# Kernel optimization log

Measured on AMD Instinct MI355X. Metric: run time of the kernel, lower is better.

Reference implementation:

```python
import jax, jax.numpy as jnp
import numpy as np

N = 100000   # nodes
E = 1600000  # edges (avg degree 16)
IN = 7       # in_channels
H = 2        # heads
C = 64       # hidden_dim (per-head channels)
NC = 4       # num_classes
SLOPE = 0.2  # PyG GATConv default negative_slope


def gat_layer(x, W, a_src, a_dst, b, src, dst, concat):
    """PyG-style GATConv. x:[n,F], W:[F,H*C], a_*:[H,C], src/dst:[E'] (incl self-loops)."""
    n = x.shape[0]
    h = (x @ W).reshape(n, H, C)                 # [n,H,C]
    es = jnp.sum(h * a_src, axis=-1)             # [n,H] per-node source score
    ed = jnp.sum(h * a_dst, axis=-1)             # [n,H] per-node dest score
    e = jax.nn.leaky_relu(es[src] + ed[dst], SLOPE)          # [E',H]
    m = jax.ops.segment_max(e, dst, num_segments=n)          # stable segment softmax
    p = jnp.exp(e - m[dst])
    s = jax.ops.segment_sum(p, dst, num_segments=n)
    alpha = p / s[dst]                                        # [E',H]
    out = jax.ops.segment_sum(h[src] * alpha[:, :, None], dst, num_segments=n)  # [n,H,C]
    out = out.reshape(n, H * C) if concat else out.mean(axis=1)
    return out + b


def setup_inputs() -> dict:
    key = jax.random.key(0)
    ks = jax.random.split(key, 14)
    sc = 0.2
    return {
        "x": jax.random.normal(ks[0], (N, IN), jnp.float32),
        "edge_index": jax.random.randint(ks[1], (2, E), 0, N, dtype=jnp.int32),
        "W1": jax.random.normal(ks[2], (IN, H * C), jnp.float32) * sc,
        "a_src1": jax.random.normal(ks[3], (H, C), jnp.float32) * sc,
        "a_dst1": jax.random.normal(ks[4], (H, C), jnp.float32) * sc,
        "b1": jnp.zeros((H * C,), jnp.float32),
        "W2": jax.random.normal(ks[5], (H * C, H * C), jnp.float32) * sc,
        "a_src2": jax.random.normal(ks[6], (H, C), jnp.float32) * sc,
        "a_dst2": jax.random.normal(ks[7], (H, C), jnp.float32) * sc,
        "b2": jnp.zeros((C,), jnp.float32),
        "Wc1": jax.random.normal(ks[8], (C, C), jnp.float32) * sc,
        "bc1": jnp.zeros((C,), jnp.float32),
        "Wc2": jax.random.normal(ks[9], (C, NC), jnp.float32) * sc,
        "bc2": jnp.zeros((NC,), jnp.float32),
    }


def reference(x, edge_index, W1, a_src1, a_dst1, b1, W2, a_src2, a_dst2, b2, Wc1, bc1, Wc2, bc2):
    loops = jnp.arange(N, dtype=edge_index.dtype)            # PyG default add_self_loops=True
    src = jnp.concatenate([edge_index[0], loops])
    dst = jnp.concatenate([edge_index[1], loops])
    h = jax.nn.relu(gat_layer(x, W1, a_src1, a_dst1, b1, src, dst, True))   # [N, 128]
    h = gat_layer(h, W2, a_src2, a_dst2, b2, src, dst, False)               # [N, 64]
    return jax.nn.relu(h @ Wc1 + bc1) @ Wc2 + bc2                           # [N, 4]
```

## Files before the change

### kernel.cpp

```cpp
#include <hip/hip_runtime.h>
#include <hip/hip_bf16.h>


#define LRELU_SLOPE 0.2f

__device__ __forceinline__ float wave_red_max(float v) {
#pragma unroll
    for (int o = 32; o > 0; o >>= 1) v = fmaxf(v, __shfl_xor(v, o));
    return v;
}
__device__ __forceinline__ float wave_red_sum(float v) {
#pragma unroll
    for (int o = 32; o > 0; o >>= 1) v += __shfl_xor(v, o);
    return v;
}
__device__ __forceinline__ float lrelu(float v) { return v > 0.f ? v : LRELU_SLOPE * v; }
__device__ __forceinline__ unsigned short f2bf(float f) {
    unsigned int x = __float_as_uint(f);
    return (unsigned short)((x + 0x7fffu + ((x >> 16) & 1u)) >> 16);
}
__device__ __forceinline__ void fma8(float* f, uint4 hv, float a) {
    unsigned u[4] = {hv.x, hv.y, hv.z, hv.w};
#pragma unroll
    for (int i = 0; i < 4; i++) {
        float lo = __uint_as_float(u[i] << 16);
        float hi = __uint_as_float(u[i] & 0xffff0000u);
        f[2 * i]     += lo * a;
        f[2 * i + 1] += hi * a;
    }
}

__global__ void k_hist(const int* __restrict__ dstA, int* __restrict__ cnt, int E) {
    int i = blockIdx.x * 256 + threadIdx.x;
    if (i < E) atomicAdd(&cnt[dstA[i]], 1);
}

__global__ void k_scan1(const int* __restrict__ cnt, int* __restrict__ rs,
                        int* __restrict__ part, int n) {
    __shared__ int sm[256];
    int t = threadIdx.x;
    int i = blockIdx.x * 256 + t;
    int v = (i < n) ? cnt[i] : 0;
    sm[t] = v;
    __syncthreads();
#pragma unroll
    for (int off = 1; off < 256; off <<= 1) {
        int x = (t >= off) ? sm[t - off] : 0;
        __syncthreads();
        sm[t] += x;
        __syncthreads();
    }
    if (i < n) rs[i] = sm[t] - v;
    if (t == 255) part[blockIdx.x] = sm[255];
}

__global__ void k_scan2(int* part, int np) {
    __shared__ int sm[512];
    int t = threadIdx.x;
    int v = (t < np) ? part[t] : 0;
    sm[t] = v;
    __syncthreads();
#pragma unroll
    for (int off = 1; off < 512; off <<= 1) {
        int x = (t >= off) ? sm[t - off] : 0;
        __syncthreads();
        sm[t] += x;
        __syncthreads();
    }
    if (t < np) part[t] = sm[t] - v;
}

__global__ void k_scan3(int* rs, const int* __restrict__ part, int n, int total) {
    int i = blockIdx.x * 256 + threadIdx.x;
    if (i < n) rs[i] += part[blockIdx.x];
    if (i == 0) rs[n] = total;
}

__global__ void k_scatter(const int* __restrict__ srcA, const int* __restrict__ dstA,
                          const int* __restrict__ rs, int* __restrict__ cur,
                          int* __restrict__ ssrc, int E) {
    int i = blockIdx.x * 256 + threadIdx.x;
    if (i < E) {
        int d = dstA[i];
        int p = atomicAdd(&cur[d], 1);
        ssrc[rs[d] + p] = srcA[i];
    }
}

__global__ void k_prep(const float* __restrict__ W1, const float* __restrict__ as1,
                       const float* __restrict__ ad1, const float* __restrict__ W2,
                       const float* __restrict__ as2, const float* __restrict__ ad2,
                       float* __restrict__ ws1, float* __restrict__ wd1,
                       float* __restrict__ ws2, float* __restrict__ wd2) {
    int t = threadIdx.x;
    int k = t >> 1, h = t & 1;
    float s = 0.f, d = 0.f;
    for (int cc = 0; cc < 64; cc++) {
        float w = W2[k * 128 + h * 64 + cc];
        s += w * as2[h * 64 + cc];
        d += w * ad2[h * 64 + cc];
    }
    ws2[t] = s;
    wd2[t] = d;
    if (t < 14) {
        int kk = t >> 1, hh = t & 1;
        float s1 = 0.f, d1 = 0.f;
        for (int cc = 0; cc < 64; cc++) {
            float w = W1[kk * 128 + hh * 64 + cc];
            s1 += w * as1[hh * 64 + cc];
            d1 += w * ad1[hh * 64 + cc];
        }
        ws1[t] = s1;
        wd1[t] = d1;
    }
}

__global__ void k_feat1(const float* __restrict__ x, const float* __restrict__ W1,
                        const float* __restrict__ ws1, const float* __restrict__ wd1,
                        unsigned short* __restrict__ h1, float* __restrict__ es1,
                        float* __restrict__ ed1, int n) {
    int node = blockIdx.x;
    int c = threadIdx.x;
    float xv[7];
#pragma unroll
    for (int k = 0; k < 7; k++) xv[k] = x[node * 7 + k];
    float acc = 0.f;
#pragma unroll
    for (int k = 0; k < 7; k++) acc += xv[k] * W1[k * 128 + c];
    h1[(size_t)node * 128 + c] = f2bf(acc);
    if (c < 2) {
        float s = 0.f;
#pragma unroll
        for (int k = 0; k < 7; k++) s += xv[k] * ws1[k * 2 + c];
        es1[node * 2 + c] = s;
    } else if (c < 4) {
        int h = c - 2;
        float s = 0.f;
#pragma unroll
        for (int k = 0; k < 7; k++) s += xv[k] * wd1[k * 2 + h];
        ed1[node * 2 + h] = s;
    }
}

__global__ void k_alpha(const float* __restrict__ es, const float* __restrict__ ed,
                        const int* __restrict__ rs, const int* __restrict__ ssrc,
                        uint4* __restrict__ rec, float2* __restrict__ aself, int n) {
    int wid = threadIdx.x >> 6, lane = threadIdx.x & 63;
    int node = blockIdx.x * 4 + wid;
    if (node >= n) return;
    int beg = rs[node], deg = rs[node + 1] - beg;
    float2 edv = *(const float2*)&ed[node * 2];
    float2 esn = *(const float2*)&es[node * 2];
    float e0s = lrelu(esn.x + edv.x);
    float e1s = lrelu(esn.y + edv.y);

    if (deg <= 64) {
        bool valid = lane < deg;
        int sv = valid ? ssrc[beg + lane] : 0;
        float2 ev; ev.x = 0.f; ev.y = 0.f;
        if (valid) ev = *(const float2*)&es[sv * 2];
        float e0 = valid ? lrelu(ev.x + edv.x) : -3.0e38f;
        float e1 = valid ? lrelu(ev.y + edv.y) : -3.0e38f;
        float m0 = fmaxf(wave_red_max(e0), e0s);
        float m1 = fmaxf(wave_red_max(e1), e1s);
        float p0 = valid ? __expf(e0 - m0) : 0.f;
        float p1 = valid ? __expf(e1 - m1) : 0.f;
        float exs0 = __expf(e0s - m0), exs1 = __expf(e1s - m1);
        float inv0 = 1.f / (wave_red_sum(p0) + exs0);
        float inv1 = 1.f / (wave_red_sum(p1) + exs1);
        if (valid)
            rec[beg + lane] = make_uint4((unsigned)sv,
                                         __float_as_uint(p0 * inv0),
                                         __float_as_uint(p1 * inv1), 0u);
        if (lane == 0) {
            float2 a; a.x = exs0 * inv0; a.y = exs1 * inv1;
            aself[node] = a;
        }
    } else {
        float m0 = e0s, s0 = 1.f, m1 = e1s, s1 = 1.f;
        for (int c0 = 0; c0 < deg; c0 += 64) {
            int i = c0 + lane;
            bool val = i < deg;
            int sv = val ? ssrc[beg + i] : 0;
            float e0 = val ? lrelu(es[sv * 2 + 0] + edv.x) : -3.0e38f;
            float e1 = val ? lrelu(es[sv * 2 + 1] + edv.y) : -3.0e38f;
            float nm0 = fmaxf(m0, wave_red_max(e0));
            float nm1 = fmaxf(m1, wave_red_max(e1));
            float p0 = val ? __expf(e0 - nm0) : 0.f;
            float p1 = val ? __expf(e1 - nm1) : 0.f;
            s0 = s0 * __expf(m0 - nm0) + wave_red_sum(p0);
            s1 = s1 * __expf(m1 - nm1) + wave_red_sum(p1);
            m0 = nm0; m1 = nm1;
        }
        float inv0 = 1.f / s0, inv1 = 1.f / s1;
        for (int c0 = 0; c0 < deg; c0 += 64) {
            int i = c0 + lane;
            if (i < deg) {
                int sv = ssrc[beg + i];
                float e0 = lrelu(es[sv * 2 + 0] + edv.x);
                float e1 = lrelu(es[sv * 2 + 1] + edv.y);
                rec[beg + i] = make_uint4((unsigned)sv,
                                          __float_as_uint(__expf(e0 - m0) * inv0),
                                          __float_as_uint(__expf(e1 - m1) * inv1), 0u);
            }
        }
        if (lane == 0) {
            float2 a; a.x = __expf(e0s - m0) * inv0; a.y = __expf(e1s - m1) * inv1;
            aself[node] = a;
        }
    }
}

template <int LAYER>
__global__ void k_aggr(const unsigned short* __restrict__ h, const int* __restrict__ rs,
                       const uint4* __restrict__ rec, const float2* __restrict__ aself,
                       const float* __restrict__ bias, float* __restrict__ out,
                       const float* __restrict__ ws2, const float* __restrict__ wd2,
                       float* __restrict__ es2, float* __restrict__ ed2,
                       const float* __restrict__ Wc1, const float* __restrict__ bc1,
                       const float* __restrict__ Wc2, const float* __restrict__ bc2,
                       int n) {
    int wid = threadIdx.x >> 6, lane = threadIdx.x & 63;
    int node = blockIdx.x * 4 + wid;
    if (node >= n) return;
    int grp = lane >> 4, sub = lane & 15;
    int base = sub * 8;
    int hd = sub >> 3;
    int beg = rs[node], deg = rs[node + 1] - beg;
    float f[8] = {0.f, 0.f, 0.f, 0.f, 0.f, 0.f, 0.f, 0.f};

    if (grp == 0) {
        float2 as = aself[node];
        float a = hd ? as.y : as.x;
        uint4 hvs = *(const uint4*)&h[(size_t)node * 128 + base];
        fma8(f, hvs, a);
    }
    int j = grp;
    for (; j + 4 < deg; j += 8) {
        uint4 r0 = rec[beg + j];
        uint4 r1 = rec[beg + j + 4];
        uint4 h0 = *(const uint4*)&h[(size_t)(int)r0.x * 128 + base];
        uint4 h1v = *(const uint4*)&h[(size_t)(int)r1.x * 128 + base];
        fma8(f, h0, hd ? __uint_as_float(r0.z) : __uint_as_float(r0.y));
        fma8(f, h1v, hd ? __uint_as_float(r1.z) : __uint_as_float(r1.y));
    }
    if (j < deg) {
        uint4 r = rec[beg + j];
        uint4 hv = *(const uint4*)&h[(size_t)(int)r.x * 128 + base];
        fma8(f, hv, hd ? __uint_as_float(r.z) : __uint_as_float(r.y));
    }

#pragma unroll
    for (int r = 0; r < 8; r++) {
        f[r] += __shfl_xor(f[r], 16);
        f[r] += __shfl_xor(f[r], 32);
    }

    if (LAYER == 1) {
        float o[8];
#pragma unroll
        for (int r = 0; r < 8; r++) o[r] = fmaxf(f[r] + bias[base + r], 0.f);
        if (grp == 0) {
            float4 v0 = {o[0], o[1], o[2], o[3]};
            float4 v1 = {o[4], o[5], o[6], o[7]};
            *(float4*)&out[(size_t)node * 128 + base] = v0;
            *(float4*)&out[(size_t)node * 128 + base + 4] = v1;
        }
        float s0 = 0.f, s1 = 0.f, d0 = 0.f, d1 = 0.f;
#pragma unroll
        for (int r = 0; r < 8; r++) {
            float2 wsv = *(const float2*)&ws2[(base + r) * 2];
            float2 wdv = *(const float2*)&wd2[(base + r) * 2];
            s0 += o[r] * wsv.x; s1 += o[r] * wsv.y;
            d0 += o[r] * wdv.x; d1 += o[r] * wdv.y;
        }
        s0 = wave_red_sum(s0) * 0.25f;
        s1 = wave_red_sum(s1) * 0.25f;
        d0 = wave_red_sum(d0) * 0.25f;
        d1 = wave_red_sum(d1) * 0.25f;
        if (lane == 0) {
            float2 sv2; sv2.x = s0; sv2.y = s1;
            float2 dv2; dv2.x = d0; dv2.y = d1;
            *(float2*)&es2[node * 2] = sv2;
            *(float2*)&ed2[node * 2] = dv2;
        }
    } else {
        float p[8];
#pragma unroll
        for (int r = 0; r < 8; r++) p[r] = __shfl_xor(f[r], 8);
        float o2[8];
#pragma unroll
        for (int r = 0; r < 8; r++)
            o2[r] = 0.5f * (f[r] + p[r]) + bias[(base & 63) + r];
        float yc = bc1[lane];
#pragma unroll
        for (int k = 0; k < 64; k++) {
            float ov = __shfl(o2[k & 7], k >> 3);
            yc += ov * Wc1[k * 64 + lane];
        }
        float y = fmaxf(yc, 0.f);
        float4 w2v = *(const float4*)&Wc2[lane * 4];
        float p0 = y * w2v.x, p1 = y * w2v.y, p2 = y * w2v.z, p3 = y * w2v.w;
        p0 = wave_red_sum(p0); p1 = wave_red_sum(p1);
        p2 = wave_red_sum(p2); p3 = wave_red_sum(p3);
        if (lane == 0) {
            float4 o; o.x = p0 + bc2[0]; o.y = p1 + bc2[1];
            o.z = p2 + bc2[2]; o.w = p3 + bc2[3];
            *(float4*)&out[(size_t)node * 4] = o;
        }
    }
}

__global__ void k_gemm2(const float* __restrict__ A, const float* __restrict__ B,
                        unsigned short* __restrict__ C, int M) {
    __shared__ float As[32][65];
    __shared__ float Bs[32][132];
    int bm = blockIdx.x * 64;
    int t = threadIdx.x;
    int tx = t & 31;
    int ty = t >> 5;
    float acc[8][4];
#pragma unroll
    for (int i = 0; i < 8; i++)
#pragma unroll
        for (int j = 0; j < 4; j++) acc[i][j] = 0.f;

    for (int k0 = 0; k0 < 128; k0 += 32) {
        int lk = t & 31, lm = t >> 5;
#pragma unroll
        for (int p = 0; p < 8; p++) {
            int m = lm + p * 8;
            int row = bm + m;
            As[lk][m] = (row < M) ? A[(size_t)row * 128 + k0 + lk] : 0.f;
        }
        int bn = t & 127, bk = t >> 7;
#pragma unroll
        for (int p = 0; p < 16; p++) {
            Bs[bk + p * 2][bn] = B[(k0 + bk + p * 2) * 128 + bn];
        }
        __syncthreads();
#pragma unroll
        for (int k = 0; k < 32; k++) {
            float a[8];
#pragma unroll
            for (int i = 0; i < 8; i++) a[i] = As[k][ty * 8 + i];
            float4 bv = *(const float4*)&Bs[k][tx * 4];
            float b[4] = {bv.x, bv.y, bv.z, bv.w};
#pragma unroll
            for (int i = 0; i < 8; i++)
#pragma unroll
                for (int j = 0; j < 4; j++) acc[i][j] += a[i] * b[j];
        }
        __syncthreads();
    }
#pragma unroll
    for (int i = 0; i < 8; i++) {
        int row = bm + ty * 8 + i;
        if (row < M) {
            ushort4 v;
            v.x = f2bf(acc[i][0]); v.y = f2bf(acc[i][1]);
            v.z = f2bf(acc[i][2]); v.w = f2bf(acc[i][3]);
            *(ushort4*)&C[(size_t)row * 128 + tx * 4] = v;
        }
    }
}

extern "C" void kernel_launch(void* const* d_in, const int* in_sizes, int n_in,
                              void* d_out, int out_size, void* d_ws, size_t ws_size,
                              hipStream_t stream) {
    const float* x   = (const float*)d_in[0];
    const int*   ei  = (const int*)d_in[1];
    const float* W1  = (const float*)d_in[2];
    const float* as1 = (const float*)d_in[3];
    const float* ad1 = (const float*)d_in[4];
    const float* b1  = (const float*)d_in[5];
    const float* W2  = (const float*)d_in[6];
    const float* as2 = (const float*)d_in[7];
    const float* ad2 = (const float*)d_in[8];
    const float* b2  = (const float*)d_in[9];
    const float* Wc1 = (const float*)d_in[10];
    const float* bc1 = (const float*)d_in[11];
    const float* Wc2 = (const float*)d_in[12];
    const float* bc2 = (const float*)d_in[13];
    float* out = (float*)d_out;

    int n = in_sizes[0] / 7;
    int E = in_sizes[1] / 2;
    const int* srcA = ei;
    const int* dstA = ei + E;

    char* ws = (char*)d_ws;
    size_t off = 0;
    auto alloc = [&](size_t bytes) -> char* {
        char* p = ws + off;
        off += (bytes + 255) & ~(size_t)255;
        return p;
    };
    unsigned short* bufH = (unsigned short*)alloc((size_t)n * 128 * 2);
    float* bufO = (float*)alloc((size_t)n * 128 * 4);
    float* es1  = (float*)alloc((size_t)n * 2 * 4);
    float* ed1  = (float*)alloc((size_t)n * 2 * 4);
    float* es2  = (float*)alloc((size_t)n * 2 * 4);
    float* ed2  = (float*)alloc((size_t)n * 2 * 4);
    float* ws1  = (float*)alloc(64);
    float* wd1  = (float*)alloc(64);
    float* ws2v = (float*)alloc(256 * 4);
    float* wd2v = (float*)alloc(256 * 4);
    int* rs   = (int*)alloc((size_t)(n + 1) * 4);
    int* cnt  = (int*)alloc((size_t)n * 4);
    int* part = (int*)alloc(512 * 4);
    int* ssrc = (int*)alloc((size_t)E * 4);
    uint4* rec = (uint4*)alloc((size_t)E * 16);
    float2* aself = (float2*)alloc((size_t)n * 8);

    int eb = (E + 255) / 256;
    int nb = (n + 255) / 256;

    hipMemsetAsync(cnt, 0, (size_t)n * 4, stream);
    k_hist<<<eb, 256, 0, stream>>>(dstA, cnt, E);
    k_scan1<<<nb, 256, 0, stream>>>(cnt, rs, part, n);
    k_scan2<<<1, 512, 0, stream>>>(part, nb);
    k_scan3<<<nb, 256, 0, stream>>>(rs, part, n, E);
    hipMemsetAsync(cnt, 0, (size_t)n * 4, stream);
    k_scatter<<<eb, 256, 0, stream>>>(srcA, dstA, rs, cnt, ssrc, E);

    k_prep<<<1, 256, 0, stream>>>(W1, as1, ad1, W2, as2, ad2, ws1, wd1, ws2v, wd2v);
    k_feat1<<<n, 128, 0, stream>>>(x, W1, ws1, wd1, bufH, es1, ed1, n);
    k_alpha<<<(n + 3) / 4, 256, 0, stream>>>(es1, ed1, rs, ssrc, rec, aself, n);
    k_aggr<1><<<(n + 3) / 4, 256, 0, stream>>>(bufH, rs, rec, aself, b1, bufO,
                                               ws2v, wd2v, es2, ed2,
                                               nullptr, nullptr, nullptr, nullptr, n);
    k_gemm2<<<(n + 63) / 64, 256, 0, stream>>>(bufO, W2, bufH, n);
    k_alpha<<<(n + 3) / 4, 256, 0, stream>>>(es2, ed2, rs, ssrc, rec, aself, n);
    k_aggr<2><<<(n + 3) / 4, 256, 0, stream>>>(bufH, rs, rec, aself, b2, out,
                                               nullptr, nullptr, nullptr, nullptr,
                                               Wc1, bc1, Wc2, bc2, n);
}
```

Baseline: 625.6 us.

## Replace per-node softmax kernel with edge-parallel exp and deferred normalization

Removes the per-node k_alpha kernel, which did max/sum wave reductions and wrote normalized alphas. An edge-parallel k_edge kernel now writes unnormalized exp(leaky_relu) weights into CSR positions that k_scatter precomputes. k_aggr accumulates the weight sums alongside the features and divides once at the end. This drops the wave reductions and the per-node launch imbalance, and k_aggr gains a deeper 16-edge unroll. The trade-off is that without max subtraction, large attention logits could overflow exp, and the extra pos array plus srcA/dstA reads are added in each layer.

After: 597.9 us. -4.4%, faster.

```diff
diff --git a/kernel.cpp b/kernel.cpp
--- a/kernel.cpp
+++ b/kernel.cpp
@@ -4,11 +4,6 @@
 
 #define LRELU_SLOPE 0.2f
 
-__device__ __forceinline__ float wave_red_max(float v) {
-#pragma unroll
-    for (int o = 32; o > 0; o >>= 1) v = fmaxf(v, __shfl_xor(v, o));
-    return v;
-}
 __device__ __forceinline__ float wave_red_sum(float v) {
 #pragma unroll
     for (int o = 32; o > 0; o >>= 1) v += __shfl_xor(v, o);
@@ -76,14 +71,13 @@
     if (i == 0) rs[n] = total;
 }
 
-__global__ void k_scatter(const int* __restrict__ srcA, const int* __restrict__ dstA,
-                          const int* __restrict__ rs, int* __restrict__ cur,
-                          int* __restrict__ ssrc, int E) {
+__global__ void k_scatter(const int* __restrict__ dstA, const int* __restrict__ rs,
+                          int* __restrict__ cur, int* __restrict__ pos, int E) {
     int i = blockIdx.x * 256 + threadIdx.x;
     if (i < E) {
         int d = dstA[i];
         int p = atomicAdd(&cur[d], 1);
-        ssrc[rs[d] + p] = srcA[i];
+        pos[i] = rs[d] + p;
     }
 }
 
@@ -142,84 +136,29 @@
     }
 }
 
-__global__ void k_alpha(const float* __restrict__ es, const float* __restrict__ ed,
-                        const int* __restrict__ rs, const int* __restrict__ ssrc,
-                        uint4* __restrict__ rec, float2* __restrict__ aself, int n) {
-    int wid = threadIdx.x >> 6, lane = threadIdx.x & 63;
-    int node = blockIdx.x * 4 + wid;
-    if (node >= n) return;
-    int beg = rs[node], deg = rs[node + 1] - beg;
-    float2 edv = *(const float2*)&ed[node * 2];
-    float2 esn = *(const float2*)&es[node * 2];
-    float e0s = lrelu(esn.x + edv.x);
-    float e1s = lrelu(esn.y + edv.y);
-
-    if (deg <= 64) {
-        bool valid = lane < deg;
-        int sv = valid ? ssrc[beg + lane] : 0;
-        float2 ev; ev.x = 0.f; ev.y = 0.f;
-        if (valid) ev = *(const float2*)&es[sv * 2];
-        float e0 = valid ? lrelu(ev.x + edv.x) : -3.0e38f;
-        float e1 = valid ? lrelu(ev.y + edv.y) : -3.0e38f;
-        float m0 = fmaxf(wave_red_max(e0), e0s);
-        float m1 = fmaxf(wave_red_max(e1), e1s);
-        float p0 = valid ? __expf(e0 - m0) : 0.f;
-        float p1 = valid ? __expf(e1 - m1) : 0.f;
-        float exs0 = __expf(e0s - m0), exs1 = __expf(e1s - m1);
-        float inv0 = 1.f / (wave_red_sum(p0) + exs0);
-        float inv1 = 1.f / (wave_red_sum(p1) + exs1);
-        if (valid)
-            rec[beg + lane] = make_uint4((unsigned)sv,
-                                         __float_as_uint(p0 * inv0),
-                                         __float_as_uint(p1 * inv1), 0u);
-        if (lane == 0) {
-            float2 a; a.x = exs0 * inv0; a.y = exs1 * inv1;
-            aself[node] = a;
-        }
-    } else {
-        float m0 = e0s, s0 = 1.f, m1 = e1s, s1 = 1.f;
-        for (int c0 = 0; c0 < deg; c0 += 64) {
-            int i = c0 + lane;
-            bool val = i < deg;
-            int sv = val ? ssrc[beg + i] : 0;
-            float e0 = val ? lrelu(es[sv * 2 + 0] + edv.x) : -3.0e38f;
-            float e1 = val ? lrelu(es[sv * 2 + 1] + edv.y) : -3.0e38f;
-            float nm0 = fmaxf(m0, wave_red_max(e0));
-            float nm1 = fmaxf(m1, wave_red_max(e1));
-            float p0 = val ? __expf(e0 - nm0) : 0.f;
-            float p1 = val ? __expf(e1 - nm1) : 0.f;
-            s0 = s0 * __expf(m0 - nm0) + wave_red_sum(p0);
-            s1 = s1 * __expf(m1 - nm1) + wave_red_sum(p1);
-            m0 = nm0; m1 = nm1;
-        }
-        float inv0 = 1.f / s0, inv1 = 1.f / s1;
-        for (int c0 = 0; c0 < deg; c0 += 64) {
-            int i = c0 + lane;
-            if (i < deg) {
-                int sv = ssrc[beg + i];
-                float e0 = lrelu(es[sv * 2 + 0] + edv.x);
-                float e1 = lrelu(es[sv * 2 + 1] + edv.y);
-                rec[beg + i] = make_uint4((unsigned)sv,
-                                          __float_as_uint(__expf(e0 - m0) * inv0),
-                                          __float_as_uint(__expf(e1 - m1) * inv1), 0u);
-            }
-        }
-        if (lane == 0) {
-            float2 a; a.x = __expf(e0s - m0) * inv0; a.y = __expf(e1s - m1) * inv1;
-            aself[node] = a;
-        }
-    }
+__global__ void k_edge(const int* __restrict__ srcA, const int* __restrict__ dstA,
+                       const int* __restrict__ pos, const float* __restrict__ es,
+                       const float* __restrict__ ed, uint4* __restrict__ rec, int E) {
+    int i = blockIdx.x * 256 + threadIdx.x;
+    if (i >= E) return;
+    int s = srcA[i], d = dstA[i];
+    float2 esv = *(const float2*)&es[s * 2];
+    float2 edv = *(const float2*)&ed[d * 2];
+    float p0 = __expf(lrelu(esv.x + edv.x));
+    float p1 = __expf(lrelu(esv.y + edv.y));
+    rec[pos[i]] = make_uint4((unsigned)s, __float_as_uint(p0),
+                             __float_as_uint(p1), 0u);
 }
 
 template <int LAYER>
 __global__ void k_aggr(const unsigned short* __restrict__ h, const int* __restrict__ rs,
-                       const uint4* __restrict__ rec, const float2* __restrict__ aself,
-                       const float* __restrict__ bias, float* __restrict__ out,
-                       const float* __restrict__ ws2, const float* __restrict__ wd2,
-                       float* __restrict__ es2, float* __restrict__ ed2,
-                       const float* __restrict__ Wc1, const float* __restrict__ bc1,
-                       const float* __restrict__ Wc2, const float* __restrict__ bc2,
-                       int n) {
+                       const uint4* __restrict__ rec, const float* __restrict__ es,
+                       const float* __restrict__ ed, const float* __restrict__ bias,
+                       float* __restrict__ out, const float* __restrict__ ws2,
+                       const float* __restrict__ wd2, float* __restrict__ es2,
+                       float* __restrict__ ed2, const float* __restrict__ Wc1,
+                       const float* __restrict__ bc1, const float* __restrict__ Wc2,
+                       const float* __restrict__ bc2, int n) {
     int wid = threadIdx.x >> 6, lane = threadIdx.x & 63;
     int node = blockIdx.x * 4 + wid;
     if (node >= n) return;
@@ -228,25 +167,51 @@
     int hd = sub >> 3;
     int beg = rs[node], deg = rs[node + 1] - beg;
     float f[8] = {0.f, 0.f, 0.f, 0.f, 0.f, 0.f, 0.f, 0.f};
-
+    float s0 = 0.f, s1 = 0.f;
+
+    float2 edv = *(const float2*)&ed[node * 2];
+    float2 esn = *(const float2*)&es[node * 2];
+    float p0s = __expf(lrelu(esn.x + edv.x));
+    float p1s = __expf(lrelu(esn.y + edv.y));
     if (grp == 0) {
-        float2 as = aself[node];
-        float a = hd ? as.y : as.x;
         uint4 hvs = *(const uint4*)&h[(size_t)node * 128 + base];
-        fma8(f, hvs, a);
+        fma8(f, hvs, hd ? p1s : p0s);
+        s0 += p0s; s1 += p1s;
     }
     int j = grp;
+    for (; j + 12 < deg; j += 16) {
+        uint4 r0 = rec[beg + j];
+        uint4 r1 = rec[beg + j + 4];
+        uint4 r2 = rec[beg + j + 8];
+        uint4 r3 = rec[beg + j + 12];
+        uint4 h0 = *(const uint4*)&h[(size_t)(int)r0.x * 128 + base];
+        uint4 h1v = *(const uint4*)&h[(size_t)(int)r1.x * 128 + base];
+        uint4 h2v = *(const uint4*)&h[(size_t)(int)r2.x * 128 + base];
+        uint4 h3v = *(const uint4*)&h[(size_t)(int)r3.x * 128 + base];
+        s0 += __uint_as_float(r0.y) + __uint_as_float(r1.y) +
+              __uint_as_float(r2.y) + __uint_as_float(r3.y);
+        s1 += __uint_as_float(r0.z) + __uint_as_float(r1.z) +
+              __uint_as_float(r2.z) + __uint_as_float(r3.z);
+        fma8(f, h0, hd ? __uint_as_float(r0.z) : __uint_as_float(r0.y));
+        fma8(f, h1v, hd ? __uint_as_float(r1.z) : __uint_as_float(r1.y));
+        fma8(f, h2v, hd ? __uint_as_float(r2.z) : __uint_as_float(r2.y));
+        fma8(f, h3v, hd ? __uint_as_float(r3.z) : __uint_as_float(r3.y));
+    }
     for (; j + 4 < deg; j += 8) {
         uint4 r0 = rec[beg + j];
         uint4 r1 = rec[beg + j + 4];
         uint4 h0 = *(const uint4*)&h[(size_t)(int)r0.x * 128 + base];
         uint4 h1v = *(const uint4*)&h[(size_t)(int)r1.x * 128 + base];
+        s0 += __uint_as_float(r0.y) + __uint_as_float(r1.y);
+        s1 += __uint_as_float(r0.z) + __uint_as_float(r1.z);
         fma8(f, h0, hd ? __uint_as_float(r0.z) : __uint_as_float(r0.y));
         fma8(f, h1v, hd ? __uint_as_float(r1.z) : __uint_as_float(r1.y));
     }
     if (j < deg) {
         uint4 r = rec[beg + j];
         uint4 hv = *(const uint4*)&h[(size_t)(int)r.x * 128 + base];
+        s0 += __uint_as_float(r.y);
+        s1 += __uint_as_float(r.z);
         fma8(f, hv, hd ? __uint_as_float(r.z) : __uint_as_float(r.y));
     }
 
@@ -255,6 +220,11 @@
         f[r] += __shfl_xor(f[r], 16);
         f[r] += __shfl_xor(f[r], 32);
     }
+    s0 += __shfl_xor(s0, 16); s0 += __shfl_xor(s0, 32);
+    s1 += __shfl_xor(s1, 16); s1 += __shfl_xor(s1, 32);
+    float scale = hd ? (1.f / s1) : (1.f / s0);
+#pragma unroll
+    for (int r = 0; r < 8; r++) f[r] *= scale;
 
     if (LAYER == 1) {
         float o[8];
@@ -266,20 +236,20 @@
             *(float4*)&out[(size_t)node * 128 + base] = v0;
             *(float4*)&out[(size_t)node * 128 + base + 4] = v1;
         }
-        float s0 = 0.f, s1 = 0.f, d0 = 0.f, d1 = 0.f;
+        float t0 = 0.f, t1 = 0.f, d0 = 0.f, d1 = 0.f;
 #pragma unroll
         for (int r = 0; r < 8; r++) {
             float2 wsv = *(const float2*)&ws2[(base + r) * 2];
             float2 wdv = *(const float2*)&wd2[(base + r) * 2];
-            s0 += o[r] * wsv.x; s1 += o[r] * wsv.y;
+            t0 += o[r] * wsv.x; t1 += o[r] * wsv.y;
             d0 += o[r] * wdv.x; d1 += o[r] * wdv.y;
         }
-        s0 = wave_red_sum(s0) * 0.25f;
-        s1 = wave_red_sum(s1) * 0.25f;
+        t0 = wave_red_sum(t0) * 0.25f;
+        t1 = wave_red_sum(t1) * 0.25f;
         d0 = wave_red_sum(d0) * 0.25f;
         d1 = wave_red_sum(d1) * 0.25f;
         if (lane == 0) {
-            float2 sv2; sv2.x = s0; sv2.y = s1;
+            float2 sv2; sv2.x = t0; sv2.y = t1;
             float2 dv2; dv2.x = d0; dv2.y = d1;
             *(float2*)&es2[node * 2] = sv2;
             *(float2*)&ed2[node * 2] = dv2;
@@ -409,9 +379,8 @@
     int* rs   = (int*)alloc((size_t)(n + 1) * 4);
     int* cnt  = (int*)alloc((size_t)n * 4);
     int* part = (int*)alloc(512 * 4);
-    int* ssrc = (int*)alloc((size_t)E * 4);
+    int* pos  = (int*)alloc((size_t)E * 4);
     uint4* rec = (uint4*)alloc((size_t)E * 16);
-    float2* aself = (float2*)alloc((size_t)n * 8);
 
     int eb = (E + 255) / 256;
     int nb = (n + 255) / 256;
@@ -422,17 +391,17 @@
     k_scan2<<<1, 512, 0, stream>>>(part, nb);
     k_scan3<<<nb, 256, 0, stream>>>(rs, part, n, E);
     hipMemsetAsync(cnt, 0, (size_t)n * 4, stream);
-    k_scatter<<<eb, 256, 0, stream>>>(srcA, dstA, rs, cnt, ssrc, E);
+    k_scatter<<<eb, 256, 0, stream>>>(dstA, rs, cnt, pos, E);
 
     k_prep<<<1, 256, 0, stream>>>(W1, as1, ad1, W2, as2, ad2, ws1, wd1, ws2v, wd2v);
     k_feat1<<<n, 128, 0, stream>>>(x, W1, ws1, wd1, bufH, es1, ed1, n);
-    k_alpha<<<(n + 3) / 4, 256, 0, stream>>>(es1, ed1, rs, ssrc, rec, aself, n);
-    k_aggr<1><<<(n + 3) / 4, 256, 0, stream>>>(bufH, rs, rec, aself, b1, bufO,
+    k_edge<<<eb, 256, 0, stream>>>(srcA, dstA, pos, es1, ed1, rec, E);
+    k_aggr<1><<<(n + 3) / 4, 256, 0, stream>>>(bufH, rs, rec, es1, ed1, b1, bufO,
                                                ws2v, wd2v, es2, ed2,
                                                nullptr, nullptr, nullptr, nullptr, n);
     k_gemm2<<<(n + 63) / 64, 256, 0, stream>>>(bufO, W2, bufH, n);
-    k_alpha<<<(n + 3) / 4, 256, 0, stream>>>(es2, ed2, rs, ssrc, rec, aself, n);
-    k_aggr<2><<<(n + 3) / 4, 256, 0, stream>>>(bufH, rs, rec, aself, b2, out,
+    k_edge<<<eb, 256, 0, stream>>>(srcA, dstA, pos, es2, ed2, rec, E);
+    k_aggr<2><<<(n + 3) / 4, 256, 0, stream>>>(bufH, rs, rec, es2, ed2, b2, out,
                                                nullptr, nullptr, nullptr, nullptr,
                                                Wc1, bc1, Wc2, bc2, n);
 }
```
